# Optimization experiments

Measured on AMD Instinct MI355X. Metric: run time of the kernel, lower is better.

The kernel has to match this reference:

```python
import jax, jax.numpy as jnp
import numpy as np

N = 50000
E = 600000
D_IN = 128
D_OUT = 128
EPS = 1e-5
LEAKY_SLOPE = 0.01


def setup_inputs() -> dict:
    key = jax.random.key(0)
    ks = jax.random.split(key, 12)
    inp = {
        "x": jax.random.normal(ks[0], (N, D_IN), dtype=jnp.float32),
        "edge_row": jax.random.randint(ks[1], (E,), 0, N, dtype=jnp.int32),
        "edge_col": jax.random.randint(ks[2], (E,), 0, N, dtype=jnp.int32),
        "edge_val": jax.random.uniform(ks[3], (E,), dtype=jnp.float32),
        # GCN params (xavier-ish scale)
        "gcn_weight": jax.random.normal(ks[4], (D_IN, D_OUT), dtype=jnp.float32) * (1.0 / np.sqrt(D_IN)),
        "gcn_bias": jax.random.normal(ks[5], (D_OUT,), dtype=jnp.float32) * 0.01,
        # LayerNorm after GCN
        "ln1_g": jnp.ones((D_OUT,), jnp.float32),
        "ln1_b": jnp.zeros((D_OUT,), jnp.float32),
        # GRUCell params (torch layout: [3H, H], gate order r,z,n)
        "W_ih": jax.random.normal(ks[6], (3 * D_OUT, D_OUT), dtype=jnp.float32) * (1.0 / np.sqrt(D_OUT)),
        "W_hh": jax.random.normal(ks[7], (3 * D_OUT, D_OUT), dtype=jnp.float32) * (1.0 / np.sqrt(D_OUT)),
        "b_ih": jax.random.normal(ks[8], (3 * D_OUT,), dtype=jnp.float32) * 0.01,
        "b_hh": jax.random.normal(ks[9], (3 * D_OUT,), dtype=jnp.float32) * 0.01,
        # LayerNorm on hidden state
        "ln2_g": jnp.ones((D_OUT,), jnp.float32),
        "ln2_b": jnp.zeros((D_OUT,), jnp.float32),
        # skip Linear: in=2*D_OUT, out=D_OUT (torch layout [out, in])
        "skip_W": jax.random.normal(ks[10], (D_OUT, 2 * D_OUT), dtype=jnp.float32) * (1.0 / np.sqrt(2 * D_OUT)),
        "skip_b": jax.random.normal(ks[11], (D_OUT,), dtype=jnp.float32) * 0.01,
        # initial RNN hidden state buffer (zeros, as in init_hidden)
        "h0": jnp.zeros((N, D_OUT), jnp.float32),
    }
    return inp


def _layer_norm(x, g, b):
    m = jnp.mean(x, axis=-1, keepdims=True)
    v = jnp.mean(jnp.square(x - m), axis=-1, keepdims=True)
    return (x - m) * jax.lax.rsqrt(v + EPS) * g + b


def reference(x, edge_row, edge_col, edge_val, gcn_weight, gcn_bias,
              ln1_g, ln1_b, W_ih, W_hh, b_ih, b_hh, ln2_g, ln2_b,
              skip_W, skip_b, h0):
    # GCN: support = x @ W; out = spmm(adj, support) + bias
    support = x @ gcn_weight                      # [N, D]
    gathered = edge_val[:, None] * support[edge_col]  # [E, D]
    agg = jax.ops.segment_sum(gathered, edge_row, num_segments=N)  # [N, D]
    xg = jax.nn.relu(agg + gcn_bias)
    xg = _layer_norm(xg, ln1_g, ln1_b)
    # GRU cell (torch semantics, gate order r, z, n)
    gi = xg @ W_ih.T + b_ih                       # [N, 3D]
    gh = h0 @ W_hh.T + b_hh                       # [N, 3D]
    i_r, i_z, i_n = jnp.split(gi, 3, axis=1)
    h_r, h_z, h_n = jnp.split(gh, 3, axis=1)
    r = jax.nn.sigmoid(i_r + h_r)
    z = jax.nn.sigmoid(i_z + h_z)
    n = jnp.tanh(i_n + r * h_n)
    h = (1.0 - z) * n + z * h0
    h = _layer_norm(h, ln2_g, ln2_b)
    # skip: concat(h, x) -> linear -> leaky_relu
    cat = jnp.concatenate([h, xg], axis=1)        # [N, 2D]
    y = cat @ skip_W.T + skip_b
    return jnp.where(y >= 0, y, LEAKY_SLOPE * y)
```

## Files before the change

### kernel.cpp

```cpp
#include <hip/hip_runtime.h>

constexpr int N = 50000;
constexpr int E = 600000;
constexpr float EPS = 1e-5f;
constexpr float SLOPE = 0.01f;
constexpr int NBLK = (N + 255) / 256;
constexpr int PRE_WPREP = 385;
constexpr int PRE_SRED  = PRE_WPREP + 32;
constexpr int PRE_HIST  = PRE_SRED + (E + 255) / 256;
constexpr int SCAT_NB = (E + 255) / 256;
constexpr int SUPP_NB = (N + 63) / 64;

typedef __attribute__((ext_vector_type(8))) short bf16x8;
typedef __attribute__((ext_vector_type(4))) float f32x4;

__device__ __forceinline__ unsigned f2bf(float f) {
    unsigned u = __float_as_uint(f);
    u += 0x7fffu + ((u >> 16) & 1u);
    return u >> 16;
}
__device__ __forceinline__ unsigned pack2(float a, float b) {
    return f2bf(a) | (f2bf(b) << 16);
}
__device__ __forceinline__ float sigm(float x) { return 1.f / (1.f + __expf(-x)); }
__device__ __forceinline__ float tanh_fast(float x) {
    return 2.f / (1.f + __expf(-2.f * x)) - 1.f;
}

__global__ __launch_bounds__(256) void k_pre(
    const float* __restrict__ gw, const float* __restrict__ wih,
    const float* __restrict__ skw, const float* __restrict__ g2,
    const float* __restrict__ b2, const float* __restrict__ skb,
    const float* __restrict__ bih, const float* __restrict__ bhh,
    const int* __restrict__ erow,
    unsigned short* __restrict__ gwT, unsigned short* __restrict__ wihb,
    unsigned short* __restrict__ skwb2, float4* __restrict__ bgate,
    float2* __restrict__ sk2, int* __restrict__ counts,
    int* __restrict__ posw) {
    const int b = blockIdx.x, t = threadIdx.x;
    if (b < PRE_WPREP) {
        const int i = b * 256 + t;
        if (i < 16384) {
            const int c = i >> 7, k = i & 127;
            gwT[i] = (unsigned short)f2bf(gw[k * 128 + c]);
        } else if (i < 65536) {
            const int o = i - 16384;
            wihb[o] = (unsigned short)f2bf(wih[o]);
        } else if (i < 98304) {
            const int o = i - 65536;
            const int k = o & 255;
            const float scale = (k < 128) ? g2[k] : 1.f;
            skwb2[o] = (unsigned short)f2bf(skw[o] * scale);
        } else if (i < 98432) {
            const int c = i - 98304;
            float4 bb;
            bb.x = bih[c] + bhh[c];
            bb.y = bih[128 + c] + bhh[128 + c];
            bb.z = bih[256 + c];
            bb.w = bhh[256 + c];
            bgate[c] = bb;
        }
    } else if (b < PRE_SRED) {
        const int wv = t >> 6, lane = t & 63;
        const int n = (b - PRE_WPREP) * 4 + wv;
        const float w0 = skw[n * 256 + lane], w1 = skw[n * 256 + 64 + lane];
        float a = w0 * g2[lane] + w1 * g2[64 + lane];
        float bb = w0 * b2[lane] + w1 * b2[64 + lane];
        for (int m = 32; m >= 1; m >>= 1) {
            a += __shfl_xor(a, m);
            bb += __shfl_xor(bb, m);
        }
        if (lane == 0) {
            float2 o;
            o.x = a;
            o.y = skb[n] + bb;
            sk2[n] = o;
        }
    } else {
        const int i = (b - PRE_SRED) * 256 + t;
        if (i < E) posw[i] = atomicAdd(&counts[erow[i]], 1);
    }
}

__global__ __launch_bounds__(256) void k_scan1(
    const int* __restrict__ counts, int* __restrict__ pre,
    int* __restrict__ bsum) {
    __shared__ int sh[256];
    const int t = threadIdx.x;
    const int i = blockIdx.x * 256 + t;
    const int v = (i < N) ? counts[i] : 0;
    sh[t] = v;
    __syncthreads();
    for (int off = 1; off < 256; off <<= 1) {
        const int u = (t >= off) ? sh[t - off] : 0;
        __syncthreads();
        sh[t] += u;
        __syncthreads();
    }
    if (i < N) pre[i] = sh[t] - v;
    if (t == 255) bsum[blockIdx.x] = sh[255];
}

__global__ __launch_bounds__(256) void k_scan2(int* __restrict__ bsum) {
    __shared__ int sh[256];
    const int t = threadIdx.x;
    const int v = (t < NBLK) ? bsum[t] : 0;
    sh[t] = v;
    __syncthreads();
    for (int off = 1; off < 256; off <<= 1) {
        const int u = (t >= off) ? sh[t - off] : 0;
        __syncthreads();
        sh[t] += u;
        __syncthreads();
    }
    if (t < NBLK) bsum[t] = sh[t] - v;
}

__global__ __launch_bounds__(256) void k_scat_supp(
    const int* __restrict__ erow, const int* __restrict__ ecol,
    const float* __restrict__ ev, const int* __restrict__ posw,
    const int* __restrict__ pre, const int* __restrict__ bsum,
    uint2* __restrict__ edge2,
    const float* __restrict__ x, const unsigned short* __restrict__ gwT,
    unsigned short* __restrict__ sup) {
    __shared__ unsigned A[64][68];
    if (blockIdx.x < SCAT_NB) {
        const int e = blockIdx.x * 256 + threadIdx.x;
        if (e < E) {
            const int row = erow[e];
            const int pos = pre[row] + bsum[row >> 8] + posw[e];
            uint2 pk;
            pk.x = (unsigned)ecol[e];
            pk.y = __float_as_uint(ev[e]);
            edge2[pos] = pk;
        }
        return;
    }
    const int t = threadIdx.x;
    const int wv = t >> 6, lane = t & 63;
    const int q = lane >> 4, ln16 = lane & 15;
    const size_t base = (size_t)(blockIdx.x - SCAT_NB) * 64;

    bf16x8 B[2][4];
#pragma unroll
    for (int i = 0; i < 2; ++i) {
        const int n = 32 * wv + 16 * i + ln16;
        const unsigned short* bp = gwT + n * 128 + q * 8;
#pragma unroll
        for (int ks = 0; ks < 4; ++ks)
            B[i][ks] = *(const bf16x8*)(bp + ks * 32);
    }
    for (int idx = t; idx < 2048; idx += 256) {
        const int r = idx >> 5, c4 = (idx & 31) * 4;
        size_t rr = base + r;
        if (rr > N - 1) rr = N - 1;
        const float4 v = *(const float4*)(x + rr * 128 + c4);
        uint2 p;
        p.x = pack2(v.x, v.y);
        p.y = pack2(v.z, v.w);
        *(uint2*)&A[r][c4 >> 1] = p;
    }
    __syncthreads();

    for (int s = 0; s < 4; ++s) {
        f32x4 C0 = {0.f, 0.f, 0.f, 0.f}, C1 = {0.f, 0.f, 0.f, 0.f};
        const unsigned short* arow = (const unsigned short*)&A[s * 16 + ln16][0];
#pragma unroll
        for (int ks = 0; ks < 4; ++ks) {
            const bf16x8 a = *(const bf16x8*)(arow + ks * 32 + q * 8);
            C0 = __builtin_amdgcn_mfma_f32_16x16x32_bf16(a, B[0][ks], C0, 0, 0, 0);
            C1 = __builtin_amdgcn_mfma_f32_16x16x32_bf16(a, B[1][ks], C1, 0, 0, 0);
        }
#pragma unroll
        for (int reg = 0; reg < 4; ++reg) {
            const size_t row = base + s * 16 + q * 4 + reg;
            if (row < N) {
                sup[row * 128 + 32 * wv + ln16] = (unsigned short)f2bf(C0[reg]);
                sup[row * 128 + 32 * wv + 16 + ln16] = (unsigned short)f2bf(C1[reg]);
            }
        }
    }
}

__global__ __launch_bounds__(256) void k_spmm_csr(
    const int* __restrict__ pre, const int* __restrict__ bsum,
    const uint2* __restrict__ edge2, const unsigned* __restrict__ sup32,
    const float* __restrict__ bias, const float* __restrict__ gam,
    const float* __restrict__ bet, unsigned* __restrict__ xg32) {
    const int wid = threadIdx.x >> 6, lane = threadIdx.x & 63;
    const int r = blockIdx.x * 4 + wid;
    const int j0 = pre[r] + bsum[r >> 8];
    const int j1 = (r + 1 < N) ? (pre[r + 1] + bsum[(r + 1) >> 8]) : E;
    float a0 = 0.f, a1 = 0.f, b0 = 0.f, b1 = 0.f;
    float c0f = 0.f, c1f = 0.f, d0 = 0.f, d1 = 0.f;
    int j = j0;
    for (; j + 3 < j1; j += 4) {
        const uint2 eA = edge2[j], eB = edge2[j + 1];
        const uint2 eC = edge2[j + 2], eD = edge2[j + 3];
        const unsigned uA = sup32[(size_t)eA.x * 64 + lane];
        const unsigned uB = sup32[(size_t)eB.x * 64 + lane];
        const unsigned uC = sup32[(size_t)eC.x * 64 + lane];
        const unsigned uD = sup32[(size_t)eD.x * 64 + lane];
        const float vA = __uint_as_float(eA.y), vB = __uint_as_float(eB.y);
        const float vC = __uint_as_float(eC.y), vD = __uint_as_float(eD.y);
        a0 += vA * __uint_as_float(uA << 16);
        a1 += vA * __uint_as_float(uA & 0xffff0000u);
        b0 += vB * __uint_as_float(uB << 16);
        b1 += vB * __uint_as_float(uB & 0xffff0000u);
        c0f += vC * __uint_as_float(uC << 16);
        c1f += vC * __uint_as_float(uC & 0xffff0000u);
        d0 += vD * __uint_as_float(uD << 16);
        d1 += vD * __uint_as_float(uD & 0xffff0000u);
    }
    for (; j < j1; ++j) {
        const uint2 eA = edge2[j];
        const unsigned uA = sup32[(size_t)eA.x * 64 + lane];
        const float vA = __uint_as_float(eA.y);
        a0 += vA * __uint_as_float(uA << 16);
        a1 += vA * __uint_as_float(uA & 0xffff0000u);
    }
    a0 += b0 + c0f + d0;
    a1 += b1 + c1f + d1;
    const int c0 = 2 * lane, c1 = c0 + 1;
    const float v0 = fmaxf(a0 + bias[c0], 0.f);
    const float v1 = fmaxf(a1 + bias[c1], 0.f);
    float s = v0 + v1, qq = v0 * v0 + v1 * v1;
    for (int m = 32; m >= 1; m >>= 1) {
        s += __shfl_xor(s, m);
        qq += __shfl_xor(qq, m);
    }
    const float mean = s * (1.f / 128.f);
    const float rstd = rsqrtf(qq * (1.f / 128.f) - mean * mean + EPS);
    const float o0 = (v0 - mean) * rstd * gam[c0] + bet[c0];
    const float o1 = (v1 - mean) * rstd * gam[c1] + bet[c1];
    xg32[(size_t)r * 64 + lane] = pack2(o0, o1);
}

__global__ __launch_bounds__(512, 4) void k_mega(
    const unsigned* __restrict__ xg32, const unsigned short* __restrict__ wihb,
    const float4* __restrict__ bgate, const unsigned short* __restrict__ skwb2,
    const float2* __restrict__ sk2, float* __restrict__ y) {
    __shared__ unsigned Axg[64][68];
    __shared__ unsigned Ah[64][68];
    __shared__ float ps[64][8], pq[64][8];
    __shared__ float lnm[64], lnr[64];
    const int t = threadIdx.x;
    const int wv = t >> 6, lane = t & 63;
    const int q = lane >> 4, ln16 = lane & 15;
    const size_t base = (size_t)blockIdx.x * 64;
    const int hc = 16 * wv + ln16;

    bf16x8 Bg[3][4];
#pragma unroll
    for (int i = 0; i < 3; ++i) {
        const unsigned short* bp = wihb + (128 * i + hc) * 128 + q * 8;
#pragma unroll
        for (int ks = 0; ks < 4; ++ks)
            Bg[i][ks] = *(const bf16x8*)(bp + ks * 32);
    }

    const float4 bg = bgate[hc];
    const float br = bg.x, bz = bg.y, bni = bg.z, bnh = bg.w;
    const float2 sk = sk2[hc];

    for (int idx = t; idx < 1024; idx += 512) {
        const int r = idx >> 4, c4 = (idx & 15) * 4;
        size_t rr = base + r;
        if (rr > N - 1) rr = N - 1;
        const uint4 v = *(const uint4*)(xg32 + rr * 64 + c4);
        *(uint4*)&Axg[r][c4] = v;
    }
    __syncthreads();

    for (int s = 0; s < 4; ++s) {
        f32x4 Cr = {0.f, 0.f, 0.f, 0.f};
        f32x4 Cz = {0.f, 0.f, 0.f, 0.f};
        f32x4 Cn = {0.f, 0.f, 0.f, 0.f};
        const unsigned short* arow = (const unsigned short*)&Axg[s * 16 + ln16][0];
#pragma unroll
        for (int ks = 0; ks < 4; ++ks) {
            const bf16x8 a = *(const bf16x8*)(arow + ks * 32 + q * 8);
            Cr = __builtin_amdgcn_mfma_f32_16x16x32_bf16(a, Bg[0][ks], Cr, 0, 0, 0);
            Cz = __builtin_amdgcn_mfma_f32_16x16x32_bf16(a, Bg[1][ks], Cz, 0, 0, 0);
            Cn = __builtin_amdgcn_mfma_f32_16x16x32_bf16(a, Bg[2][ks], Cn, 0, 0, 0);
        }
#pragma unroll
        for (int reg = 0; reg < 4; ++reg) {
            const int lrow = s * 16 + q * 4 + reg;
            const float r = sigm(Cr[reg] + br);
            const float z = sigm(Cz[reg] + bz);
            const float h = (1.f - z) * tanh_fast(Cn[reg] + bni + r * bnh);
            ((unsigned short*)&Ah[lrow][0])[hc] = (unsigned short)f2bf(h);
            float p = h, qs = h * h;
            p += __shfl_xor(p, 1);
            qs += __shfl_xor(qs, 1);
            p += __shfl_xor(p, 2);
            qs += __shfl_xor(qs, 2);
            p += __shfl_xor(p, 4);
            qs += __shfl_xor(qs, 4);
            p += __shfl_xor(p, 8);
            qs += __shfl_xor(qs, 8);
            if (ln16 == 0) {
                ps[lrow][wv] = p;
                pq[lrow][wv] = qs;
            }
        }
    }
    bf16x8 Bs[8];
#pragma unroll
    for (int ks = 0; ks < 8; ++ks)
        Bs[ks] = *(const bf16x8*)(skwb2 + hc * 256 + ks * 32 + q * 8);
    __syncthreads();
    if (t < 64) {
        float s = 0.f, qq = 0.f;
#pragma unroll
        for (int i = 0; i < 8; ++i) {
            s += ps[t][i];
            qq += pq[t][i];
        }
        const float mean = s * (1.f / 128.f);
        lnm[t] = mean;
        lnr[t] = rsqrtf(qq * (1.f / 128.f) - mean * mean + EPS);
    }
    __syncthreads();
    for (int s = 0; s < 4; ++s) {
        f32x4 Ch = {0.f, 0.f, 0.f, 0.f};
        f32x4 Cx = {0.f, 0.f, 0.f, 0.f};
        const unsigned short* ah = (const unsigned short*)&Ah[s * 16 + ln16][0];
        const unsigned short* ax = (const unsigned short*)&Axg[s * 16 + ln16][0];
#pragma unroll
        for (int ks = 0; ks < 4; ++ks) {
            const bf16x8 a = *(const bf16x8*)(ah + ks * 32 + q * 8);
            Ch = __builtin_amdgcn_mfma_f32_16x16x32_bf16(a, Bs[ks], Ch, 0, 0, 0);
        }
#pragma unroll
        for (int ks = 0; ks < 4; ++ks) {
            const bf16x8 a = *(const bf16x8*)(ax + ks * 32 + q * 8);
            Cx = __builtin_amdgcn_mfma_f32_16x16x32_bf16(a, Bs[4 + ks], Cx, 0, 0, 0);
        }
#pragma unroll
        for (int reg = 0; reg < 4; ++reg) {
            const int lrow = s * 16 + q * 4 + reg;
            const size_t row = base + lrow;
            if (row < N) {
                const float m = lnm[lrow], rs = lnr[lrow];
                const float v = rs * (Ch[reg] - m * sk.x) + Cx[reg] + sk.y;
                y[row * 128 + hc] = v >= 0.f ? v : SLOPE * v;
            }
        }
    }
}

extern "C" void kernel_launch(void* const* d_in, const int* in_sizes, int n_in,
                              void* d_out, int out_size, void* d_ws, size_t ws_size,
                              hipStream_t stream) {
    const float* x     = (const float*)d_in[0];
    const int*   erow  = (const int*)d_in[1];
    const int*   ecol  = (const int*)d_in[2];
    const float* ev    = (const float*)d_in[3];
    const float* gcn_w = (const float*)d_in[4];
    const float* gcn_b = (const float*)d_in[5];
    const float* ln1g  = (const float*)d_in[6];
    const float* ln1b  = (const float*)d_in[7];
    const float* wih   = (const float*)d_in[8];
    const float* bih   = (const float*)d_in[10];
    const float* bhh   = (const float*)d_in[11];
    const float* ln2g  = (const float*)d_in[12];
    const float* ln2b  = (const float*)d_in[13];
    const float* skw   = (const float*)d_in[14];
    const float* skb   = (const float*)d_in[15];
    float* y = (float*)d_out;

    char* p = (char*)d_ws;
    unsigned short* sup  = (unsigned short*)p;  p += (size_t)N * 128 * 2;
    unsigned* xg32       = (unsigned*)p;        p += (size_t)N * 64 * 4;
    uint2* edge2         = (uint2*)p;           p += (size_t)E * 8;
    int* posw            = (int*)p;             p += (size_t)E * 4;
    int* counts          = (int*)p;             p += (size_t)N * 4;
    int* pre             = (int*)p;             p += (size_t)N * 4;
    int* bsum            = (int*)p;             p += (size_t)NBLK * 4;
    unsigned short* gwT  = (unsigned short*)p;  p += 16384 * 2;
    unsigned short* wihb = (unsigned short*)p;  p += 49152 * 2;
    unsigned short* skwb2= (unsigned short*)p;  p += 32768 * 2;
    float4* bgate        = (float4*)p;          p += 128 * 16;
    float2* sk2          = (float2*)p;          p += 128 * 8;

    hipMemsetAsync(counts, 0, (size_t)N * sizeof(int), stream);
    k_pre<<<PRE_HIST, 256, 0, stream>>>(gcn_w, wih, skw, ln2g, ln2b, skb,
                                        bih, bhh, erow, gwT, wihb, skwb2,
                                        bgate, sk2, counts, posw);
    k_scan1<<<NBLK, 256, 0, stream>>>(counts, pre, bsum);
    k_scan2<<<1, 256, 0, stream>>>(bsum);
    k_scat_supp<<<SCAT_NB + SUPP_NB, 256, 0, stream>>>(
        erow, ecol, ev, posw, pre, bsum, edge2, x, gwT, sup);
    k_spmm_csr<<<N / 4, 256, 0, stream>>>(pre, bsum, edge2, (const unsigned*)sup,
                                          gcn_b, ln1g, ln1b, xg32);
    k_mega<<<(N + 63) / 64, 512, 0, stream>>>(xg32, wihb, bgate, skwb2, sk2, y);
}
```

Baseline: 245.5 us.

## Drop posw buffer via atomicSub ranks, use HIP bf16 converts, recompute LN2 stats

```diff
diff --git a/kernel.cpp b/kernel.cpp
--- a/kernel.cpp
+++ b/kernel.cpp
@@ -1,4 +1,5 @@
 #include <hip/hip_runtime.h>
+#include <hip/hip_bf16.h>
 
 constexpr int N = 50000;
 constexpr int E = 600000;
@@ -19,12 +20,28 @@
     u += 0x7fffu + ((u >> 16) & 1u);
     return u >> 16;
 }
-__device__ __forceinline__ unsigned pack2(float a, float b) {
-    return f2bf(a) | (f2bf(b) << 16);
+__device__ __forceinline__ unsigned cvt_pair(float a, float b) {
+    float2 f; f.x = a; f.y = b;
+    __hip_bfloat162 h2 = __float22bfloat162_rn(f);
+    unsigned u;
+    __builtin_memcpy(&u, &h2, 4);
+    return u;
+}
+__device__ __forceinline__ unsigned short cvt1(float a) {
+    __hip_bfloat16 h = __float2bfloat16(a);
+    unsigned short u;
+    __builtin_memcpy(&u, &h, 2);
+    return u;
 }
 __device__ __forceinline__ float sigm(float x) { return 1.f / (1.f + __expf(-x)); }
 __device__ __forceinline__ float tanh_fast(float x) {
     return 2.f / (1.f + __expf(-2.f * x)) - 1.f;
+}
+__device__ __forceinline__ void acc2(unsigned u, float& s, float& q) {
+    const float lo = __uint_as_float(u << 16);
+    const float hi = __uint_as_float(u & 0xffff0000u);
+    s += lo + hi;
+    q += lo * lo + hi * hi;
 }
 
 __global__ __launch_bounds__(256) void k_pre(
@@ -35,8 +52,7 @@
     const int* __restrict__ erow,
     unsigned short* __restrict__ gwT, unsigned short* __restrict__ wihb,
     unsigned short* __restrict__ skwb2, float4* __restrict__ bgate,
-    float2* __restrict__ sk2, int* __restrict__ counts,
-    int* __restrict__ posw) {
+    float2* __restrict__ sk2, int* __restrict__ counts) {
     const int b = blockIdx.x, t = threadIdx.x;
     if (b < PRE_WPREP) {
         const int i = b * 256 + t;
@@ -78,7 +94,7 @@
         }
     } else {
         const int i = (b - PRE_SRED) * 256 + t;
-        if (i < E) posw[i] = atomicAdd(&counts[erow[i]], 1);
+        if (i < E) atomicAdd(&counts[erow[i]], 1);
     }
 }
 
@@ -118,7 +134,7 @@
 
 __global__ __launch_bounds__(256) void k_scat_supp(
     const int* __restrict__ erow, const int* __restrict__ ecol,
-    const float* __restrict__ ev, const int* __restrict__ posw,
+    const float* __restrict__ ev, int* __restrict__ counts,
     const int* __restrict__ pre, const int* __restrict__ bsum,
     uint2* __restrict__ edge2,
     const float* __restrict__ x, const unsigned short* __restrict__ gwT,
@@ -128,7 +144,8 @@
         const int e = blockIdx.x * 256 + threadIdx.x;
         if (e < E) {
             const int row = erow[e];
-            const int pos = pre[row] + bsum[row >> 8] + posw[e];
+            const int rank = atomicSub(&counts[row], 1) - 1;
+            const int pos = pre[row] + bsum[row >> 8] + rank;
             uint2 pk;
             pk.x = (unsigned)ecol[e];
             pk.y = __float_as_uint(ev[e]);
@@ -156,8 +173,8 @@
         if (rr > N - 1) rr = N - 1;
         const float4 v = *(const float4*)(x + rr * 128 + c4);
         uint2 p;
-        p.x = pack2(v.x, v.y);
-        p.y = pack2(v.z, v.w);
+        p.x = cvt_pair(v.x, v.y);
+        p.y = cvt_pair(v.z, v.w);
         *(uint2*)&A[r][c4 >> 1] = p;
     }
     __syncthreads();
@@ -175,8 +192,8 @@
         for (int reg = 0; reg < 4; ++reg) {
             const size_t row = base + s * 16 + q * 4 + reg;
             if (row < N) {
-                sup[row * 128 + 32 * wv + ln16] = (unsigned short)f2bf(C0[reg]);
-                sup[row * 128 + 32 * wv + 16 + ln16] = (unsigned short)f2bf(C1[reg]);
+                sup[row * 128 + 32 * wv + ln16] = cvt1(C0[reg]);
+                sup[row * 128 + 32 * wv + 16 + ln16] = cvt1(C1[reg]);
             }
         }
     }
@@ -233,7 +250,7 @@
     const float rstd = rsqrtf(qq * (1.f / 128.f) - mean * mean + EPS);
     const float o0 = (v0 - mean) * rstd * gam[c0] + bet[c0];
     const float o1 = (v1 - mean) * rstd * gam[c1] + bet[c1];
-    xg32[(size_t)r * 64 + lane] = pack2(o0, o1);
+    xg32[(size_t)r * 64 + lane] = cvt_pair(o0, o1);
 }
 
 __global__ __launch_bounds__(512, 4) void k_mega(
@@ -242,7 +259,6 @@
     const float2* __restrict__ sk2, float* __restrict__ y) {
     __shared__ unsigned Axg[64][68];
     __shared__ unsigned Ah[64][68];
-    __shared__ float ps[64][8], pq[64][8];
     __shared__ float lnm[64], lnr[64];
     const int t = threadIdx.x;
     const int wv = t >> 6, lane = t & 63;
@@ -290,20 +306,7 @@
             const float r = sigm(Cr[reg] + br);
             const float z = sigm(Cz[reg] + bz);
             const float h = (1.f - z) * tanh_fast(Cn[reg] + bni + r * bnh);
-            ((unsigned short*)&Ah[lrow][0])[hc] = (unsigned short)f2bf(h);
-            float p = h, qs = h * h;
-            p += __shfl_xor(p, 1);
-            qs += __shfl_xor(qs, 1);
-            p += __shfl_xor(p, 2);
-            qs += __shfl_xor(qs, 2);
-            p += __shfl_xor(p, 4);
-            qs += __shfl_xor(qs, 4);
-            p += __shfl_xor(p, 8);
-            qs += __shfl_xor(qs, 8);
-            if (ln16 == 0) {
-                ps[lrow][wv] = p;
-                pq[lrow][wv] = qs;
-            }
+            ((unsigned short*)&Ah[lrow][0])[hc] = cvt1(h);
         }
     }
     bf16x8 Bs[8];
@@ -311,18 +314,25 @@
     for (int ks = 0; ks < 8; ++ks)
         Bs[ks] = *(const bf16x8*)(skwb2 + hc * 256 + ks * 32 + q * 8);
     __syncthreads();
-    if (t < 64) {
+
+    {
+        const int row = t >> 3, sub = t & 7;
+        const uint4 a = *(const uint4*)&Ah[row][sub * 8];
+        const uint4 b = *(const uint4*)&Ah[row][sub * 8 + 4];
         float s = 0.f, qq = 0.f;
-#pragma unroll
-        for (int i = 0; i < 8; ++i) {
-            s += ps[t][i];
-            qq += pq[t][i];
-        }
-        const float mean = s * (1.f / 128.f);
-        lnm[t] = mean;
-        lnr[t] = rsqrtf(qq * (1.f / 128.f) - mean * mean + EPS);
-    }
-    __syncthreads();
+        acc2(a.x, s, qq); acc2(a.y, s, qq); acc2(a.z, s, qq); acc2(a.w, s, qq);
+        acc2(b.x, s, qq); acc2(b.y, s, qq); acc2(b.z, s, qq); acc2(b.w, s, qq);
+        s += __shfl_xor(s, 1); qq += __shfl_xor(qq, 1);
+        s += __shfl_xor(s, 2); qq += __shfl_xor(qq, 2);
+        s += __shfl_xor(s, 4); qq += __shfl_xor(qq, 4);
+        if (sub == 0) {
+            const float mean = s * (1.f / 128.f);
+            lnm[row] = mean;
+            lnr[row] = rsqrtf(qq * (1.f / 128.f) - mean * mean + EPS);
+        }
+    }
+    __syncthreads();
+
     for (int s = 0; s < 4; ++s) {
         f32x4 Ch = {0.f, 0.f, 0.f, 0.f};
         f32x4 Cx = {0.f, 0.f, 0.f, 0.f};
@@ -331,12 +341,9 @@
 #pragma unroll
         for (int ks = 0; ks < 4; ++ks) {
             const bf16x8 a = *(const bf16x8*)(ah + ks * 32 + q * 8);
+            const bf16x8 b = *(const bf16x8*)(ax + ks * 32 + q * 8);
             Ch = __builtin_amdgcn_mfma_f32_16x16x32_bf16(a, Bs[ks], Ch, 0, 0, 0);
-        }
-#pragma unroll
-        for (int ks = 0; ks < 4; ++ks) {
-            const bf16x8 a = *(const bf16x8*)(ax + ks * 32 + q * 8);
-            Cx = __builtin_amdgcn_mfma_f32_16x16x32_bf16(a, Bs[4 + ks], Cx, 0, 0, 0);
+            Cx = __builtin_amdgcn_mfma_f32_16x16x32_bf16(b, Bs[4 + ks], Cx, 0, 0, 0);
         }
 #pragma unroll
         for (int reg = 0; reg < 4; ++reg) {
@@ -375,7 +382,6 @@
     unsigned short* sup  = (unsigned short*)p;  p += (size_t)N * 128 * 2;
     unsigned* xg32       = (unsigned*)p;        p += (size_t)N * 64 * 4;
     uint2* edge2         = (uint2*)p;           p += (size_t)E * 8;
-    int* posw            = (int*)p;             p += (size_t)E * 4;
     int* counts          = (int*)p;             p += (size_t)N * 4;
     int* pre             = (int*)p;             p += (size_t)N * 4;
     int* bsum            = (int*)p;             p += (size_t)NBLK * 4;
@@ -388,11 +394,11 @@
     hipMemsetAsync(counts, 0, (size_t)N * sizeof(int), stream);
     k_pre<<<PRE_HIST, 256, 0, stream>>>(gcn_w, wih, skw, ln2g, ln2b, skb,
                                         bih, bhh, erow, gwT, wihb, skwb2,
-                                        bgate, sk2, counts, posw);
+                                        bgate, sk2, counts);
     k_scan1<<<NBLK, 256, 0, stream>>>(counts, pre, bsum);
     k_scan2<<<1, 256, 0, stream>>>(bsum);
     k_scat_supp<<<SCAT_NB + SUPP_NB, 256, 0, stream>>>(
-        erow, ecol, ev, posw, pre, bsum, edge2, x, gwT, sup);
+        erow, ecol, ev, counts, pre, bsum, edge2, x, gwT, sup);
     k_spmm_csr<<<N / 4, 256, 0, stream>>>(pre, bsum, edge2, (const unsigned*)sup,
                                           gcn_b, ln1g, ln1b, xg32);
     k_mega<<<(N + 63) / 64, 512, 0, stream>>>(xg32, wihb, bgate, skwb2, sk2, y);
```

Result: slower. 257.2 us (+4.8%).
